# Kernel tuning notes

Measured on AMD Instinct MI355X. Metric: run time of the kernel, lower is better.

Reference implementation:

```python
import jax, jax.numpy as jnp
import numpy as np

NUM_HEADS = 8
EPS = 1e-5  # torch GroupNorm default eps


def setup_inputs() -> dict:
    key = jax.random.key(0)
    ks = jax.random.split(key, 3)
    B, C, H, W = 8, 384, 32, 32
    x = jax.random.normal(ks[0], (B, C, H, W), dtype=jnp.float32)
    qkv_w = jax.random.normal(ks[1], (3 * C, C), dtype=jnp.float32) * 0.02
    proj_w = jax.random.normal(ks[2], (C, C), dtype=jnp.float32) * 0.02
    proj_b = jnp.zeros((C,), dtype=jnp.float32)
    lambda_param = jnp.ones((1, NUM_HEADS, 1, 1), dtype=jnp.float32) * 0.5
    gc = NUM_HEADS * ((C // NUM_HEADS) // 2)  # 192 group-norm channels
    gn_weight = jnp.ones((gc,), dtype=jnp.float32)
    gn_bias = jnp.zeros((gc,), dtype=jnp.float32)
    return {"x": x, "qkv_w": qkv_w, "lambda_param": lambda_param,
            "gn_weight": gn_weight, "gn_bias": gn_bias,
            "proj_w": proj_w, "proj_b": proj_b}


def reference(x, qkv_w, lambda_param, gn_weight, gn_bias, proj_w, proj_b):
    B, C, H, W = x.shape
    nh = NUM_HEADS
    hd = C // nh
    hd2 = hd // 2
    N = H * W
    scale = hd ** -0.5

    xf = x.reshape(B, C, N)
    qkv = jnp.einsum('oc,bcn->bon', qkv_w, xf)  # (B, 3C, N), 1x1 conv no bias
    q, k, v = jnp.split(qkv, 3, axis=1)
    q = q.reshape(B, nh, hd, N)
    k = k.reshape(B, nh, hd, N)
    v = v.reshape(B, nh, hd, N)

    q1, q2 = q[:, :, :hd2], q[:, :, hd2:]
    k1, k2 = k[:, :, :hd2], k[:, :, hd2:]
    v1, v2 = v[:, :, :hd2], v[:, :, hd2:]

    # GroupNorm(2 groups) on q2 viewed as (B, nh*hd2, H, W)
    gc = nh * hd2
    qg = q2.reshape(B, 2, (gc // 2) * N)  # normalize over (group channels, H, W)
    mean = qg.mean(axis=2, keepdims=True)
    var = qg.var(axis=2, keepdims=True)
    qg = (qg - mean) * jax.lax.rsqrt(var + EPS)
    q2n = qg.reshape(B, gc, N) * gn_weight[None, :, None] + gn_bias[None, :, None]
    q2n = q2n.reshape(B, nh, hd2, N)

    # dual softmax attention maps (B, nh, N, N)
    attn1 = jax.nn.softmax(jnp.einsum('bhdn,bhdm->bhnm', q1, k1) * scale, axis=-1)
    attn2 = jax.nn.softmax(jnp.einsum('bhdn,bhdm->bhnm', q2n, k2) * scale * lambda_param, axis=-1)
    diff = attn1 - attn2

    out1 = jnp.einsum('bhnm,bhdm->bhnd', diff, v1)  # (B, nh, N, hd2)
    out2 = jnp.einsum('bhnm,bhdm->bhnd', diff, v2)
    out = jnp.concatenate([out1, out2], axis=2)  # (B, nh, 2N, hd2) -- matches torch cat dim=2
    out = out.reshape(B, C, H, W)

    out = jnp.einsum('oc,bchw->bohw', proj_w, out) + proj_b[None, :, None, None]
    return out
```

## Files before the change

### kernel.cpp

```cpp
#include <hip/hip_runtime.h>
#include <hip/hip_bf16.h>
#include <stdint.h>

typedef _Float16 half8 __attribute__((ext_vector_type(8)));
typedef _Float16 half4 __attribute__((ext_vector_type(4)));
typedef __fp16 fp16x2 __attribute__((ext_vector_type(2)));
typedef float floatx4 __attribute__((ext_vector_type(4)));
typedef float floatx16 __attribute__((ext_vector_type(16)));

#define SCALE 0.14433756729740643f
#define LOG2E 1.4426950408889634f


__device__ inline float fexp2(float x) { return __builtin_exp2f(x); }

__device__ inline uint32_t pkrtz(float a, float b) {
  fp16x2 h = __builtin_amdgcn_cvt_pkrtz(a, b);
  union { fp16x2 h; uint32_t u; } cv; cv.h = h; return cv.u;
}

__launch_bounds__(256)
__global__ void k_prep(const float* __restrict__ qkv_w, const float* __restrict__ pw,
                       const float* __restrict__ x, _Float16* __restrict__ Wf,
                       _Float16* __restrict__ PWf, _Float16* __restrict__ Xt) {
  const int bid = blockIdx.x;
  if (bid < 288) {
    const float* src = (bid < 216) ? qkv_w : pw;
    _Float16* dst = (bid < 216) ? Wf : PWf;
    int cid = (bid < 216 ? bid : bid - 216) * 256 + threadIdx.x;
    int nchunks = (bid < 216) ? 55296 : 18432;
    if (cid >= nchunks) return;
    int lane = cid & 63;
    int t = cid >> 6;
    int cb = t % 12;
    int g16 = t / 12;
    const float* s = src + (long)(g16 * 16 + (lane & 15)) * 384 + cb * 32 + (lane >> 4) * 8;
    floatx4 a = *(const floatx4*)s;
    floatx4 b = *(const floatx4*)(s + 4);
    half8 h;
    #pragma unroll
    for (int j = 0; j < 4; j++) { h[j] = (_Float16)a[j]; h[j+4] = (_Float16)b[j]; }
    *(half8*)(dst + (long)cid * 8) = h;
  } else {
    int idx = bid - 288;
    const int cblk = idx % 12, nseg = (idx / 12) & 3, b = idx / 48;
    const float* S = x + ((long)b * 384 + cblk * 32) * 1024 + nseg * 256;
    _Float16* D = Xt + (long)b * 393216 + cblk * 32768 + (long)nseg * 256 * 32;
    __shared__ _Float16 T[32][264];
    const int wv = threadIdx.x >> 6, lane = threadIdx.x & 63;
    #pragma unroll
    for (int rr = 0; rr < 8; rr++) {
      int r = wv * 8 + rr;
      floatx4 v = *(const floatx4*)(S + (long)r * 1024 + lane * 4);
      half4 h;
      #pragma unroll
      for (int j = 0; j < 4; j++) h[j] = (_Float16)v[j];
      *(half4*)&T[r][lane * 4] = h;
    }
    __syncthreads();
    const int nn = threadIdx.x >> 3, c = (threadIdx.x & 7) * 4;
    #pragma unroll
    for (int p = 0; p < 8; p++) {
      int n = p * 32 + nn;
      half4 h;
      #pragma unroll
      for (int i = 0; i < 4; i++) h[i] = T[c + i][n];
      *(half4*)(D + (long)n * 32 + c) = h;
    }
  }
}

__launch_bounds__(256)
__global__ void k_trh(const _Float16* __restrict__ src, _Float16* __restrict__ dst) {
  const int cblk = blockIdx.x, nseg = blockIdx.y, b = blockIdx.z;
  const _Float16* S = src + ((long)b * 384 + cblk * 32) * 1024 + nseg * 256;
  _Float16* D = dst + (long)b * 393216 + cblk * 32768 + (long)nseg * 256 * 32;
  __shared__ _Float16 T[32][264];
  const int wv = threadIdx.x >> 6, lane = threadIdx.x & 63;
  #pragma unroll
  for (int rr = 0; rr < 8; rr++) {
    int r = wv * 8 + rr;
    *(half4*)&T[r][lane * 4] = *(const half4*)(S + (long)r * 1024 + lane * 4);
  }
  __syncthreads();
  const int nn = threadIdx.x >> 3, c = (threadIdx.x & 7) * 4;
  #pragma unroll
  for (int p = 0; p < 8; p++) {
    int n = p * 32 + nn;
    half4 h;
    #pragma unroll
    for (int i = 0; i < 4; i++) h[i] = T[c + i][n];
    *(half4*)(D + (long)n * 32 + c) = h;
  }
}

__launch_bounds__(256, 4)
__global__ void k_qkv(const _Float16* __restrict__ Xt, const _Float16* __restrict__ Wf,
                      _Float16* __restrict__ Qs, _Float16* __restrict__ Ks,
                      _Float16* __restrict__ Vs, float* __restrict__ gnpart) {
  const int tid = threadIdx.x;
  const int lane = tid & 63;
  const int wv = tid >> 6;
  const int l15 = lane & 15;
  const int g = lane >> 4;
  const int o0 = blockIdx.x * 48;
  const int n0 = blockIdx.y * 64;
  const int b = blockIdx.z;

  __shared__ __align__(16) _Float16 WA[18432];
  __shared__ float red[8];

  {
    const _Float16* wsrc = Wf + ((long)blockIdx.x * 36 + wv * 9) * 512 + lane * 8;
    uint4 wtmp[9];
    #pragma unroll
    for (int k = 0; k < 9; k++) wtmp[k] = *(const uint4*)(wsrc + k * 512);
    #pragma unroll
    for (int k = 0; k < 9; k++) *(uint4*)(&WA[(wv * 9 + k) * 512 + lane * 8]) = wtmp[k];
  }

  const int ncol = n0 + wv * 16 + l15;
  const _Float16* xp = Xt + (long)b * 393216 + (long)ncol * 32 + g * 8;
  half8 xb[12];
  #pragma unroll
  for (int cb = 0; cb < 12; cb++) xb[cb] = *(const half8*)(xp + cb * 32768);

  __syncthreads();

  floatx4 zero4 = {0.f, 0.f, 0.f, 0.f};
  floatx4 acc0 = zero4, acc1 = zero4, acc2 = zero4;

  #pragma unroll
  for (int cb = 0; cb < 12; cb++) {
    half8 a0 = *(const half8*)&WA[(cb) * 512 + lane * 8];
    half8 a1 = *(const half8*)&WA[(12 + cb) * 512 + lane * 8];
    half8 a2 = *(const half8*)&WA[(24 + cb) * 512 + lane * 8];
    acc0 = __builtin_amdgcn_mfma_f32_16x16x32_f16(a0, xb[cb], acc0, 0, 0, 0);
    acc1 = __builtin_amdgcn_mfma_f32_16x16x32_f16(a1, xb[cb], acc1, 0, 0, 0);
    acc2 = __builtin_amdgcn_mfma_f32_16x16x32_f16(a2, xb[cb], acc2, 0, 0, 0);
  }

  floatx4 acc[3] = {acc0, acc1, acc2};
  __syncthreads();
  _Float16* T = WA;

  if (o0 < 768) {
    #pragma unroll
    for (int rt = 0; rt < 3; rt++)
      #pragma unroll
      for (int r = 0; r < 4; r++)
        T[(wv * 16 + l15) * 52 + rt * 16 + g * 4 + r] = (_Float16)acc[rt][r];
    __syncthreads();
    const int qk = o0 >= 384;
    const int hh = (o0 - qk * 384) / 48;
    _Float16* base = (qk ? Ks : Qs) + (long)(b * 8 + hh) * 65536;
    #pragma unroll
    for (int it = 0; it < 2; it++) {
      int slot = it * 256 + tid;
      int ntl = slot >> 8;
      int t   = (slot >> 6) & 3;
      int ln  = slot & 63;
      int hi_s = ln >> 5, l31_s = ln & 31;
      int n_ = ntl * 32 + l31_s;
      int c0 = t * 16 + hi_s * 8;
      half8 val;
      #pragma unroll
      for (int j = 0; j < 8; j++) {
        int col = c0 + j;
        int d48 = col < 24 ? col : col - 8;
        bool isq = (col < 24) || (col >= 32 && col < 56);
        val[j] = isq ? T[n_ * 52 + d48] : (_Float16)0;
      }
      *(half8*)(base + ((((n0 >> 5) + ntl) * 4 + t) * 64 + ln) * 8) = val;
    }
    if (!qk) {
      float s1 = 0.f, s2 = 0.f;
      int n_ = tid >> 2, k0 = (tid & 3) * 6;
      #pragma unroll
      for (int k = 0; k < 6; k++) {
        float v = (float)T[n_ * 52 + 24 + k0 + k];
        s1 += v; s2 += v * v;
      }
      #pragma unroll
      for (int off = 32; off > 0; off >>= 1) {
        s1 += __shfl_down(s1, off);
        s2 += __shfl_down(s2, off);
      }
      if ((tid & 63) == 0) { red[tid >> 6] = s1; red[4 + (tid >> 6)] = s2; }
      __syncthreads();
      if (tid == 0) {
        int slot = (b * 8 + hh) * 16 + (n0 >> 6);
        gnpart[slot * 2]     = red[0] + red[1] + red[2] + red[3];
        gnpart[slot * 2 + 1] = red[4] + red[5] + red[6] + red[7];
      }
    }
  } else {
    #pragma unroll
    for (int rt = 0; rt < 3; rt++)
      #pragma unroll
      for (int r = 0; r < 4; r++)
        T[(rt * 16 + g * 4 + r) * 72 + wv * 16 + l15] = (_Float16)acc[rt][r];
    __syncthreads();
    const int hh = (o0 - 768) / 48;
    _Float16* base = Vs + (long)(b * 8 + hh) * 65536;
    #pragma unroll
    for (int it = 0; it < 2; it++) {
      int slot = it * 256 + tid;
      int lwin = slot >> 8;
      int ckc  = (slot >> 6) & 3;
      int kc   = ckc & 1, c = ckc >> 1;
      int ln = slot & 63;
      int hi_s = ln >> 5, l31_s = ln & 31;
      int d48 = c * 32 + l31_s;
      half8 val;
      if (d48 < 48) {
        int mb = lwin * 32 + kc * 16 + hi_s * 4;
        half4 a = *(const half4*)&T[d48 * 72 + mb];
        half4 bq = *(const half4*)&T[d48 * 72 + mb + 8];
        val[0] = a[0]; val[1] = a[1]; val[2] = a[2]; val[3] = a[3];
        val[4] = bq[0]; val[5] = bq[1]; val[6] = bq[2]; val[7] = bq[3];
      } else {
        _Float16 f = (d48 == 48) ? (_Float16)1 : (_Float16)0;
        #pragma unroll
        for (int j = 0; j < 8; j++) val[j] = f;
      }
      *(half8*)(base + ((((n0 >> 5) + lwin) * 4 + ckc) * 64 + ln) * 8) = val;
    }
  }
}

__launch_bounds__(512, 4)
__global__ void k_attn(const _Float16* __restrict__ Qs, const _Float16* __restrict__ Ks,
                       const _Float16* __restrict__ Vs, const float* __restrict__ gnpart,
                       const float* __restrict__ lam, const float* __restrict__ gw,
                       const float* __restrict__ gb, _Float16* __restrict__ Yf) {
  const int tid = threadIdx.x;
  const int lane = tid & 63;
  const int wv = tid >> 6;
  const int l31 = lane & 31;
  const int hi = lane >> 5;
  const int id = blockIdx.x;
  const int bh = ((id >> 6) << 3) | (id & 7);
  const int ntlgrp = (id >> 3) & 7;
  const int br = wv & 1;
  const int ntile = ntlgrp * 4 + (wv >> 1);
  const int n0 = ntile * 32;
  const int b = bh >> 3, h = bh & 7;

  const _Float16* Qp = Qs + (long)bh * 65536 + (ntile * 256 + lane) * 8;
  half8 qra = *(const half8*)(Qp + (2 * br) * 512);
  half8 qrb = *(const half8*)(Qp + (2 * br + 1) * 512);
  half8 qfa, qfb;
  if (br == 0) {
    const float s1s = SCALE * LOG2E;
    #pragma unroll
    for (int j = 0; j < 8; j++) {
      qfa[j] = (_Float16)((float)qra[j] * s1s);
      qfb[j] = (_Float16)((float)qrb[j] * s1s);
    }
  } else {
    const int grp = h >> 2;
    const float* pp = gnpart + (b * 128 + grp * 64) * 2;
    float S1 = pp[lane * 2], S2 = pp[lane * 2 + 1];
    #pragma unroll
    for (int off = 1; off < 64; off <<= 1) {
      S1 += __shfl_xor(S1, off);
      S2 += __shfl_xor(S2, off);
    }
    float mean = S1 * (1.f / 98304.f);
    float rstd = rsqrtf(S2 * (1.f / 98304.f) - mean * mean + 1e-5f);
    float sl = SCALE * LOG2E * lam[h];
    const float* gwp = gw + h * 24;
    const float* gbp = gb + h * 24;
    #pragma unroll
    for (int j = 0; j < 8; j++) {
      qfa[j] = (_Float16)((((float)qra[j] - mean) * rstd * gwp[hi * 8 + j] + gbp[hi * 8 + j]) * sl);
      qfb[j] = (_Float16)((((float)qrb[j] - mean) * rstd * gwp[16 + j] + gbp[16 + j]) * sl);
    }
  }

  const _Float16* gK = Ks + (long)bh * 65536 + ((wv >> 2) * 2048 + (wv & 3) * 512) + lane * 8;
  const _Float16* gV = Vs + (long)bh * 65536 + ((wv >> 2) * 2048 + (wv & 3) * 512) + lane * 8;

  __shared__ __align__(16) char smem[32768];
  const int ldsK = wv * 1024 + lane * 16;
  const int ldsV = 8192 + wv * 1024 + lane * 16;

  floatx16 z16;
  #pragma unroll
  for (int i = 0; i < 16; i++) z16[i] = 0.f;
  floatx16 accA = z16, accB = z16;

  {
    uint4 a = *(const uint4*)gK;
    uint4 c = *(const uint4*)gV;
    *(uint4*)(smem + ldsK) = a;
    *(uint4*)(smem + ldsV) = c;
  }
  __syncthreads();

  #pragma unroll 2
  for (int i = 0; i < 16; i++) {
    const int cur = (i & 1) << 14;
    uint4 sa, sc;
    if (i < 15) {
      sa = *(const uint4*)(gK + (i + 1) * 4096);
      sc = *(const uint4*)(gV + (i + 1) * 4096);
    }
    #pragma unroll
    for (int j = 0; j < 2; j++) {
      const char* Kb = smem + cur + j * 4096;
      const char* Vb = smem + cur + 8192 + j * 4096;
      half8 kfa = *(const half8*)(Kb + (2 * br) * 1024 + lane * 16);
      half8 kfb = *(const half8*)(Kb + (2 * br + 1) * 1024 + lane * 16);

      floatx16 s = __builtin_amdgcn_mfma_f32_32x32x16_f16(kfa, qfa, z16, 0, 0, 0);
      s = __builtin_amdgcn_mfma_f32_32x32x16_f16(kfb, qfb, s, 0, 0, 0);

      half8 vf0 = *(const half8*)(Vb + lane * 16);
      half8 vf1 = *(const half8*)(Vb + 1024 + lane * 16);
      half8 vf2 = *(const half8*)(Vb + 2048 + lane * 16);
      half8 vf3 = *(const half8*)(Vb + 3072 + lane * 16);

      uint32_t u[8];
      #pragma unroll
      for (int q = 0; q < 8; q++)
        u[q] = pkrtz(fexp2(s[2 * q]), fexp2(s[2 * q + 1]));

      union { uint32_t u[4]; half8 h; } pa;
      pa.u[0] = u[0]; pa.u[1] = u[1]; pa.u[2] = u[2]; pa.u[3] = u[3];
      half8 pc0 = pa.h;
      pa.u[0] = u[4]; pa.u[1] = u[5]; pa.u[2] = u[6]; pa.u[3] = u[7];
      half8 pc1 = pa.h;

      accA = __builtin_amdgcn_mfma_f32_32x32x16_f16(pc0, vf0, accA, 0, 0, 0);
      accA = __builtin_amdgcn_mfma_f32_32x32x16_f16(pc1, vf1, accA, 0, 0, 0);
      accB = __builtin_amdgcn_mfma_f32_32x32x16_f16(pc0, vf2, accB, 0, 0, 0);
      accB = __builtin_amdgcn_mfma_f32_32x32x16_f16(pc1, vf3, accB, 0, 0, 0);
    }
    if (i < 15) {
      *(uint4*)(smem + (cur ^ 16384) + ldsK) = sa;
      *(uint4*)(smem + (cur ^ 16384) + ldsV) = sc;
    }
    __syncthreads();
  }

  const int pairid = wv >> 1;
  float* rbuf = (float*)(smem + pairid * 8192);
  if (br == 1) {
    #pragma unroll
    for (int r = 0; r < 16; r++) {
      rbuf[r * 64 + lane] = accA[r];
      rbuf[(16 + r) * 64 + lane] = accB[r];
    }
  }
  __syncthreads();
  if (br == 0) {
    float a2a[16], a2b[16];
    #pragma unroll
    for (int r = 0; r < 16; r++) {
      a2a[r] = rbuf[r * 64 + lane];
      a2b[r] = rbuf[(16 + r) * 64 + lane];
    }
    _Float16* Ybh = Yf + (long)bh * 49152;
    const int src = (lane & 32) + 16;
    #pragma unroll
    for (int r = 0; r < 16; r++) {
      float i1 = __builtin_amdgcn_rcpf(__shfl(accB[r], src));
      float i2 = __builtin_amdgcn_rcpf(__shfl(a2b[r], src));
      int n = n0 + (r & 3) + 8 * ((r >> 2) & 3) + 4 * hi;
      float o0 = accA[r] * i1 - a2a[r] * i2;
      float o1 = accB[r] * i1 - a2b[r] * i2;
      int p0 = l31 >= 24;
      Ybh[p0 * 24576 + n * 24 + (l31 - p0 * 24)] = (_Float16)o0;
      if (l31 < 16) Ybh[24576 + n * 24 + 8 + l31] = (_Float16)o1;
    }
  }
}

__launch_bounds__(256, 4)
__global__ void k_proj(const _Float16* __restrict__ Yt, const _Float16* __restrict__ PWf,
                       const float* __restrict__ PB, float* __restrict__ out) {
  const int tid = threadIdx.x, lane = tid & 63, wv = tid >> 6, l15 = lane & 15, g = lane >> 4;
  const int o0 = blockIdx.x * 64, m0 = blockIdx.y * 64, b = blockIdx.z;

  __shared__ __align__(16) _Float16 PA[24576];

  {
    const _Float16* psrc = PWf + ((long)blockIdx.x * 48 + wv * 12) * 512 + lane * 8;
    uint4 ptmp[12];
    #pragma unroll
    for (int k = 0; k < 12; k++) ptmp[k] = *(const uint4*)(psrc + k * 512);
    #pragma unroll
    for (int k = 0; k < 12; k++) *(uint4*)(&PA[(wv * 12 + k) * 512 + lane * 8]) = ptmp[k];
  }

  const int mcol = m0 + wv * 16 + l15;
  const _Float16* yp = Yt + (long)b * 393216 + (long)mcol * 32 + g * 8;
  half8 yb[12];
  #pragma unroll
  for (int cb = 0; cb < 12; cb++) yb[cb] = *(const half8*)(yp + cb * 32768);

  __syncthreads();

  floatx4 zero4 = {0.f, 0.f, 0.f, 0.f};
  floatx4 acc0 = zero4, acc1 = zero4, acc2 = zero4, acc3 = zero4;

  #pragma unroll
  for (int cb = 0; cb < 12; cb++) {
    half8 a0 = *(const half8*)&PA[(cb) * 512 + lane * 8];
    half8 a1 = *(const half8*)&PA[(12 + cb) * 512 + lane * 8];
    half8 a2 = *(const half8*)&PA[(24 + cb) * 512 + lane * 8];
    half8 a3 = *(const half8*)&PA[(36 + cb) * 512 + lane * 8];
    acc0 = __builtin_amdgcn_mfma_f32_16x16x32_f16(a0, yb[cb], acc0, 0, 0, 0);
    acc1 = __builtin_amdgcn_mfma_f32_16x16x32_f16(a1, yb[cb], acc1, 0, 0, 0);
    acc2 = __builtin_amdgcn_mfma_f32_16x16x32_f16(a2, yb[cb], acc2, 0, 0, 0);
    acc3 = __builtin_amdgcn_mfma_f32_16x16x32_f16(a3, yb[cb], acc3, 0, 0, 0);
  }

  floatx4 acc[4] = {acc0, acc1, acc2, acc3};
  #pragma unroll
  for (int rt = 0; rt < 4; rt++) {
    int o_ = o0 + rt * 16 + g * 4;
    #pragma unroll
    for (int r = 0; r < 4; r++) {
      out[(long)(b * 384 + o_ + r) * 1024 + mcol] = acc[rt][r] + PB[o_ + r];
    }
  }
}

extern "C" void kernel_launch(void* const* d_in, const int* in_sizes, int n_in,
                              void* d_out, int out_size, void* d_ws, size_t ws_size,
                              hipStream_t stream) {
  const float* x     = (const float*)d_in[0];
  const float* qkv_w = (const float*)d_in[1];
  const float* lam   = (const float*)d_in[2];
  const float* gw    = (const float*)d_in[3];
  const float* gb    = (const float*)d_in[4];
  const float* pw    = (const float*)d_in[5];
  const float* pb    = (const float*)d_in[6];
  float* out = (float*)d_out;
  char* ws = (char*)d_ws;
  _Float16* Qs  = (_Float16*)ws;
  _Float16* Ks  = (_Float16*)(ws + 8388608);
  _Float16* Vs  = (_Float16*)(ws + 16777216);
  float* gnpart   = (float*)(ws + 25165824);
  _Float16* Yf  = (_Float16*)(ws + 26214400);
  _Float16* Xt  = (_Float16*)(ws + 37752832);
  _Float16* Yt  = (_Float16*)(ws + 44044288);
  _Float16* Wf  = (_Float16*)(ws + 50335744);
  _Float16* PWf = (_Float16*)(ws + 51220480);

  hipLaunchKernelGGL(k_prep,    dim3(672),        dim3(256), 0, stream, qkv_w, pw, x, Wf, PWf, Xt);
  hipLaunchKernelGGL(k_qkv,     dim3(24, 16, 8),  dim3(256), 0, stream, Xt, Wf, Qs, Ks, Vs, gnpart);
  hipLaunchKernelGGL(k_attn,    dim3(512),        dim3(512), 0, stream, Qs, Ks, Vs, gnpart, lam, gw, gb, Yf);
  hipLaunchKernelGGL(k_trh,     dim3(12, 4, 8),   dim3(256), 0, stream, Yf, Yt);
  hipLaunchKernelGGL(k_proj,    dim3(6, 16, 8),   dim3(256), 0, stream, Yt, PWf, pb, out);
}
```

Before: 85.35 us.

## Compute both attention branches per wave, halving block size in attention kernel

Each wave now computes both softmax branches (plain and group-normalized q) for its query tile, instead of splitting them across a pair of waves. This removes the shared-memory exchange and extra barrier that used to combine the two branches, and reuses each V fragment for both branches. Blocks shrink from 512 to 256 threads, and each thread now loads two K/V chunks per stage. In exchange, each wave holds twice as many accumulators (more registers), and each block has fewer waves to hide latency.

```diff
diff --git a/kernel.cpp b/kernel.cpp
--- a/kernel.cpp
+++ b/kernel.cpp
@@ -229,7 +229,7 @@
   }
 }
 
-__launch_bounds__(512, 4)
+__launch_bounds__(256, 2)
 __global__ void k_attn(const _Float16* __restrict__ Qs, const _Float16* __restrict__ Ks,
                        const _Float16* __restrict__ Vs, const float* __restrict__ gnpart,
                        const float* __restrict__ lam, const float* __restrict__ gw,
@@ -242,23 +242,23 @@
   const int id = blockIdx.x;
   const int bh = ((id >> 6) << 3) | (id & 7);
   const int ntlgrp = (id >> 3) & 7;
-  const int br = wv & 1;
-  const int ntile = ntlgrp * 4 + (wv >> 1);
+  const int ntile = ntlgrp * 4 + wv;
   const int n0 = ntile * 32;
   const int b = bh >> 3, h = bh & 7;
 
   const _Float16* Qp = Qs + (long)bh * 65536 + (ntile * 256 + lane) * 8;
-  half8 qra = *(const half8*)(Qp + (2 * br) * 512);
-  half8 qrb = *(const half8*)(Qp + (2 * br + 1) * 512);
-  half8 qfa, qfb;
-  if (br == 0) {
+  half8 qr0a = *(const half8*)(Qp);
+  half8 qr0b = *(const half8*)(Qp + 512);
+  half8 qr1a = *(const half8*)(Qp + 1024);
+  half8 qr1b = *(const half8*)(Qp + 1536);
+  half8 qf0a, qf0b, qf1a, qf1b;
+  {
     const float s1s = SCALE * LOG2E;
     #pragma unroll
     for (int j = 0; j < 8; j++) {
-      qfa[j] = (_Float16)((float)qra[j] * s1s);
-      qfb[j] = (_Float16)((float)qrb[j] * s1s);
-    }
-  } else {
+      qf0a[j] = (_Float16)((float)qr0a[j] * s1s);
+      qf0b[j] = (_Float16)((float)qr0b[j] * s1s);
+    }
     const int grp = h >> 2;
     const float* pp = gnpart + (b * 128 + grp * 64) * 2;
     float S1 = pp[lane * 2], S2 = pp[lane * 2 + 1];
@@ -269,108 +269,115 @@
     }
     float mean = S1 * (1.f / 98304.f);
     float rstd = rsqrtf(S2 * (1.f / 98304.f) - mean * mean + 1e-5f);
-    float sl = SCALE * LOG2E * lam[h];
+    float sl = s1s * lam[h];
     const float* gwp = gw + h * 24;
     const float* gbp = gb + h * 24;
     #pragma unroll
     for (int j = 0; j < 8; j++) {
-      qfa[j] = (_Float16)((((float)qra[j] - mean) * rstd * gwp[hi * 8 + j] + gbp[hi * 8 + j]) * sl);
-      qfb[j] = (_Float16)((((float)qrb[j] - mean) * rstd * gwp[16 + j] + gbp[16 + j]) * sl);
-    }
-  }
-
-  const _Float16* gK = Ks + (long)bh * 65536 + ((wv >> 2) * 2048 + (wv & 3) * 512) + lane * 8;
-  const _Float16* gV = Vs + (long)bh * 65536 + ((wv >> 2) * 2048 + (wv & 3) * 512) + lane * 8;
+      qf1a[j] = (_Float16)((((float)qr1a[j] - mean) * rstd * gwp[hi * 8 + j] + gbp[hi * 8 + j]) * sl);
+      qf1b[j] = (_Float16)((((float)qr1b[j] - mean) * rstd * gwp[16 + j] + gbp[16 + j]) * sl);
+    }
+  }
+
+  const _Float16* gK = Ks + (long)bh * 65536 + wv * 1024 + lane * 8;
+  const _Float16* gV = Vs + (long)bh * 65536 + wv * 1024 + lane * 8;
 
   __shared__ __align__(16) char smem[32768];
-  const int ldsK = wv * 1024 + lane * 16;
-  const int ldsV = 8192 + wv * 1024 + lane * 16;
+  const int ldsK0 = wv * 2048 + lane * 16;
+  const int ldsV0 = 8192 + wv * 2048 + lane * 16;
 
   floatx16 z16;
   #pragma unroll
   for (int i = 0; i < 16; i++) z16[i] = 0.f;
-  floatx16 accA = z16, accB = z16;
+  floatx16 acc1A = z16, acc1B = z16, acc2A = z16, acc2B = z16;
 
   {
-    uint4 a = *(const uint4*)gK;
-    uint4 c = *(const uint4*)gV;
-    *(uint4*)(smem + ldsK) = a;
-    *(uint4*)(smem + ldsV) = c;
+    uint4 k0 = *(const uint4*)gK;
+    uint4 k1 = *(const uint4*)(gK + 512);
+    uint4 v0 = *(const uint4*)gV;
+    uint4 v1 = *(const uint4*)(gV + 512);
+    *(uint4*)(smem + ldsK0) = k0;
+    *(uint4*)(smem + ldsK0 + 1024) = k1;
+    *(uint4*)(smem + ldsV0) = v0;
+    *(uint4*)(smem + ldsV0 + 1024) = v1;
   }
   __syncthreads();
 
   #pragma unroll 2
   for (int i = 0; i < 16; i++) {
     const int cur = (i & 1) << 14;
-    uint4 sa, sc;
+    uint4 sk0, sk1, sv0, sv1;
     if (i < 15) {
-      sa = *(const uint4*)(gK + (i + 1) * 4096);
-      sc = *(const uint4*)(gV + (i + 1) * 4096);
+      sk0 = *(const uint4*)(gK + (i + 1) * 4096);
+      sk1 = *(const uint4*)(gK + (i + 1) * 4096 + 512);
+      sv0 = *(const uint4*)(gV + (i + 1) * 4096);
+      sv1 = *(const uint4*)(gV + (i + 1) * 4096 + 512);
     }
     #pragma unroll
     for (int j = 0; j < 2; j++) {
       const char* Kb = smem + cur + j * 4096;
       const char* Vb = smem + cur + 8192 + j * 4096;
-      half8 kfa = *(const half8*)(Kb + (2 * br) * 1024 + lane * 16);
-      half8 kfb = *(const half8*)(Kb + (2 * br + 1) * 1024 + lane * 16);
-
-      floatx16 s = __builtin_amdgcn_mfma_f32_32x32x16_f16(kfa, qfa, z16, 0, 0, 0);
-      s = __builtin_amdgcn_mfma_f32_32x32x16_f16(kfb, qfb, s, 0, 0, 0);
+      half8 kf0a = *(const half8*)(Kb + lane * 16);
+      half8 kf0b = *(const half8*)(Kb + 1024 + lane * 16);
+      half8 kf1a = *(const half8*)(Kb + 2048 + lane * 16);
+      half8 kf1b = *(const half8*)(Kb + 3072 + lane * 16);
+
+      floatx16 s1 = __builtin_amdgcn_mfma_f32_32x32x16_f16(kf0a, qf0a, z16, 0, 0, 0);
+      s1 = __builtin_amdgcn_mfma_f32_32x32x16_f16(kf0b, qf0b, s1, 0, 0, 0);
+      floatx16 s2 = __builtin_amdgcn_mfma_f32_32x32x16_f16(kf1a, qf1a, z16, 0, 0, 0);
+      s2 = __builtin_amdgcn_mfma_f32_32x32x16_f16(kf1b, qf1b, s2, 0, 0, 0);
 
       half8 vf0 = *(const half8*)(Vb + lane * 16);
       half8 vf1 = *(const half8*)(Vb + 1024 + lane * 16);
       half8 vf2 = *(const half8*)(Vb + 2048 + lane * 16);
       half8 vf3 = *(const half8*)(Vb + 3072 + lane * 16);
 
-      uint32_t u[8];
-      #pragma unroll
-      for (int q = 0; q < 8; q++)
-        u[q] = pkrtz(fexp2(s[2 * q]), fexp2(s[2 * q + 1]));
+      uint32_t u1[8], u2[8];
+      #pragma unroll
+      for (int q = 0; q < 8; q++) {
+        u1[q] = pkrtz(fexp2(s1[2 * q]), fexp2(s1[2 * q + 1]));
+        u2[q] = pkrtz(fexp2(s2[2 * q]), fexp2(s2[2 * q + 1]));
+      }
 
       union { uint32_t u[4]; half8 h; } pa;
-      pa.u[0] = u[0]; pa.u[1] = u[1]; pa.u[2] = u[2]; pa.u[3] = u[3];
-      half8 pc0 = pa.h;
-      pa.u[0] = u[4]; pa.u[1] = u[5]; pa.u[2] = u[6]; pa.u[3] = u[7];
-      half8 pc1 = pa.h;
-
-      accA = __builtin_amdgcn_mfma_f32_32x32x16_f16(pc0, vf0, accA, 0, 0, 0);
-      accA = __builtin_amdgcn_mfma_f32_32x32x16_f16(pc1, vf1, accA, 0, 0, 0);
-      accB = __builtin_amdgcn_mfma_f32_32x32x16_f16(pc0, vf2, accB, 0, 0, 0);
-      accB = __builtin_amdgcn_mfma_f32_32x32x16_f16(pc1, vf3, accB, 0, 0, 0);
+      pa.u[0] = u1[0]; pa.u[1] = u1[1]; pa.u[2] = u1[2]; pa.u[3] = u1[3];
+      half8 p1c0 = pa.h;
+      pa.u[0] = u1[4]; pa.u[1] = u1[5]; pa.u[2] = u1[6]; pa.u[3] = u1[7];
+      half8 p1c1 = pa.h;
+      pa.u[0] = u2[0]; pa.u[1] = u2[1]; pa.u[2] = u2[2]; pa.u[3] = u2[3];
+      half8 p2c0 = pa.h;
+      pa.u[0] = u2[4]; pa.u[1] = u2[5]; pa.u[2] = u2[6]; pa.u[3] = u2[7];
+      half8 p2c1 = pa.h;
+
+      acc1A = __builtin_amdgcn_mfma_f32_32x32x16_f16(p1c0, vf0, acc1A, 0, 0, 0);
+      acc1A = __builtin_amdgcn_mfma_f32_32x32x16_f16(p1c1, vf1, acc1A, 0, 0, 0);
+      acc1B = __builtin_amdgcn_mfma_f32_32x32x16_f16(p1c0, vf2, acc1B, 0, 0, 0);
+      acc1B = __builtin_amdgcn_mfma_f32_32x32x16_f16(p1c1, vf3, acc1B, 0, 0, 0);
+      acc2A = __builtin_amdgcn_mfma_f32_32x32x16_f16(p2c0, vf0, acc2A, 0, 0, 0);
+      acc2A = __builtin_amdgcn_mfma_f32_32x32x16_f16(p2c1, vf1, acc2A, 0, 0, 0);
+      acc2B = __builtin_amdgcn_mfma_f32_32x32x16_f16(p2c0, vf2, acc2B, 0, 0, 0);
+      acc2B = __builtin_amdgcn_mfma_f32_32x32x16_f16(p2c1, vf3, acc2B, 0, 0, 0);
     }
     if (i < 15) {
-      *(uint4*)(smem + (cur ^ 16384) + ldsK) = sa;
-      *(uint4*)(smem + (cur ^ 16384) + ldsV) = sc;
+      const int nxt = cur ^ 16384;
+      *(uint4*)(smem + nxt + ldsK0) = sk0;
+      *(uint4*)(smem + nxt + ldsK0 + 1024) = sk1;
+      *(uint4*)(smem + nxt + ldsV0) = sv0;
+      *(uint4*)(smem + nxt + ldsV0 + 1024) = sv1;
     }
     __syncthreads();
   }
 
-  const int pairid = wv >> 1;
-  float* rbuf = (float*)(smem + pairid * 8192);
-  if (br == 1) {
-    #pragma unroll
-    for (int r = 0; r < 16; r++) {
-      rbuf[r * 64 + lane] = accA[r];
-      rbuf[(16 + r) * 64 + lane] = accB[r];
-    }
-  }
-  __syncthreads();
-  if (br == 0) {
-    float a2a[16], a2b[16];
-    #pragma unroll
-    for (int r = 0; r < 16; r++) {
-      a2a[r] = rbuf[r * 64 + lane];
-      a2b[r] = rbuf[(16 + r) * 64 + lane];
-    }
+  {
     _Float16* Ybh = Yf + (long)bh * 49152;
     const int src = (lane & 32) + 16;
     #pragma unroll
     for (int r = 0; r < 16; r++) {
-      float i1 = __builtin_amdgcn_rcpf(__shfl(accB[r], src));
-      float i2 = __builtin_amdgcn_rcpf(__shfl(a2b[r], src));
+      float i1 = __builtin_amdgcn_rcpf(__shfl(acc1B[r], src));
+      float i2 = __builtin_amdgcn_rcpf(__shfl(acc2B[r], src));
       int n = n0 + (r & 3) + 8 * ((r >> 2) & 3) + 4 * hi;
-      float o0 = accA[r] * i1 - a2a[r] * i2;
-      float o1 = accB[r] * i1 - a2b[r] * i2;
+      float o0 = acc1A[r] * i1 - acc2A[r] * i2;
+      float o1 = acc1B[r] * i1 - acc2B[r] * i2;
       int p0 = l31 >= 24;
       Ybh[p0 * 24576 + n * 24 + (l31 - p0 * 24)] = (_Float16)o0;
       if (l31 < 16) Ybh[24576 + n * 24 + 8 + l31] = (_Float16)o1;
@@ -453,7 +460,7 @@
 
   hipLaunchKernelGGL(k_prep,    dim3(672),        dim3(256), 0, stream, qkv_w, pw, x, Wf, PWf, Xt);
   hipLaunchKernelGGL(k_qkv,     dim3(24, 16, 8),  dim3(256), 0, stream, Xt, Wf, Qs, Ks, Vs, gnpart);
-  hipLaunchKernelGGL(k_attn,    dim3(512),        dim3(512), 0, stream, Qs, Ks, Vs, gnpart, lam, gw, gb, Yf);
+  hipLaunchKernelGGL(k_attn,    dim3(512),        dim3(256), 0, stream, Qs, Ks, Vs, gnpart, lam, gw, gb, Yf);
   hipLaunchKernelGGL(k_trh,     dim3(12, 4, 8),   dim3(256), 0, stream, Yf, Yt);
   hipLaunchKernelGGL(k_proj,    dim3(6, 16, 8),   dim3(256), 0, stream, Yt, PWf, pb, out);
 }
```

New measurement: 83.95 us, median of 2. No clear change (-1.6%).
